# Optimization experiments

Measured on AMD Instinct MI355X. Metric: run time of the kernel, lower is better.

Reference implementation:

```python
import jax, jax.numpy as jnp
import numpy as np

D_MODEL = 1024
NHEAD = 16
HEAD_DIM = D_MODEL // NHEAD
B, S = 4, 2048
NEG_INF = -1000000000.0


def setup_inputs() -> dict:
    key = jax.random.key(0)
    ks = jax.random.split(key, 12)
    s = 1.0 / np.sqrt(D_MODEL)
    inp = {
        "query": jax.random.normal(ks[0], (B, S, D_MODEL), jnp.float32),
        "key": jax.random.normal(ks[1], (B, S, D_MODEL), jnp.float32),
        "value": jax.random.normal(ks[2], (B, S, D_MODEL), jnp.float32),
        # causal mask: 1 = attend, 0 = blocked
        "mask": jnp.broadcast_to(jnp.tril(jnp.ones((S, S), jnp.int32)), (B, S, S)),
        "Wq": jax.random.normal(ks[3], (D_MODEL, D_MODEL), jnp.float32) * s,
        "bq": jnp.zeros((D_MODEL,), jnp.float32),
        "Wk": jax.random.normal(ks[4], (D_MODEL, D_MODEL), jnp.float32) * s,
        "bk": jnp.zeros((D_MODEL,), jnp.float32),
        "Wv": jax.random.normal(ks[5], (D_MODEL, D_MODEL), jnp.float32) * s,
        "bv": jnp.zeros((D_MODEL,), jnp.float32),
        "Wo": jax.random.normal(ks[6], (D_MODEL, D_MODEL), jnp.float32) * s,
        "bo": jnp.zeros((D_MODEL,), jnp.float32),
    }
    return inp


def reference(query, key, value, mask, Wq, bq, Wk, bk, Wv, bv, Wo, bo):
    b, sq, d = query.shape
    scale = np.float32(1.0 / np.sqrt(HEAD_DIM))

    def proj(x, W, bias):
        # nn.Linear: x @ W.T + b, then split heads -> [b, H, s, hd]
        y = jnp.einsum('bsd,ed->bse', x, W) + bias
        return y.reshape(b, -1, NHEAD, HEAD_DIM).transpose(0, 2, 1, 3)

    q = proj(query, Wq, bq)
    k = proj(key, Wk, bk)
    v = proj(value, Wv, bv)

    scores = jnp.einsum('bhqd,bhkd->bhqk', q, k) * scale  # [b,H,sq,sk]
    scores = jnp.where(mask[:, None, :, :] == 0, jnp.float32(NEG_INF), scores)
    attn = jax.nn.softmax(scores, axis=-1)  # dropout p=0 -> identity
    out = jnp.einsum('bhqk,bhkd->bhqd', attn, v)
    out = out.transpose(0, 2, 1, 3).reshape(b, sq, d)
    return jnp.einsum('bsd,ed->bse', out, Wo) + bo
```

## Files before the change

kernel.cpp:

```cpp
#include <hip/hip_runtime.h>
#include <stdint.h>

#define D_MODEL 1024
#define NHEAD   16
#define BATCH   4
#define SEQ     2048
#define M_TOTAL 8192
#define R_ELEMS ((size_t)M_TOTAL * D_MODEL)
#define W_ELEMS ((size_t)D_MODEL * D_MODEL)

typedef short bf8_t __attribute__((ext_vector_type(8)));
typedef float f4_t  __attribute__((ext_vector_type(4)));

#define MFMA16(a, b, c) __builtin_amdgcn_mfma_f32_16x16x32_bf16(a, b, c, 0, 0, 0)

#define SCALE_LOG2E 0.1803368801111244f

#define M_FIX 20.0f

__device__ __forceinline__ unsigned short f2b(float f) {
    union { float f; unsigned int u; } v; v.f = f;
    return (unsigned short)((v.u + 0x7fffu + ((v.u >> 16) & 1u)) >> 16);
}
__device__ __forceinline__ unsigned short f2b_fast(float f) {
    union { float f; unsigned int u; } v; v.f = f;
    return (unsigned short)((v.u + 0x8000u) >> 16);
}

#if __has_builtin(__builtin_amdgcn_exp2f)
#define EXP2(x) __builtin_amdgcn_exp2f(x)
#else
#define EXP2(x) exp2f(x)
#endif

__device__ __forceinline__ void async16(const unsigned short* g, unsigned short* l) {
    __builtin_amdgcn_global_load_lds(
        (const __attribute__((address_space(1))) unsigned int*)g,
        (__attribute__((address_space(3))) unsigned int*)l, 16, 0, 0);
}

__device__ __forceinline__ void cvt_store8(const float* __restrict__ g, unsigned short* l) {
    const float4 x = *(const float4*)g;
    const float4 y = *(const float4*)(g + 4);
    unsigned short t[8] = { f2b(x.x), f2b(x.y), f2b(x.z), f2b(x.w),
                            f2b(y.x), f2b(y.y), f2b(y.z), f2b(y.w) };
    *(uint4*)l = *(const uint4*)t;
}

__global__ __launch_bounds__(256)
void cvt_w(const float* __restrict__ s0, const float* __restrict__ s1,
           const float* __restrict__ s2, const float* __restrict__ s3,
           unsigned short* __restrict__ d) {
    const unsigned int gid = blockIdx.x * 256 + threadIdx.x;
    const unsigned int t = gid >> 17, i = gid & ((1u << 17) - 1);
    const float* s = (t == 0 ? s0 : t == 1 ? s1 : t == 2 ? s2 : s3) + (size_t)i * 8;
    unsigned short* d2 = d + (size_t)t * W_ELEMS + (size_t)i * 8;
    const float4 x = *(const float4*)s;
    const float4 y = *(const float4*)(s + 4);
    unsigned short o[8] = { f2b(x.x), f2b(x.y), f2b(x.z), f2b(x.w),
                            f2b(y.x), f2b(y.y), f2b(y.z), f2b(y.w) };
    *(uint4*)d2 = *(const uint4*)o;
}

template<int AF32, int WF32>
__device__ __forceinline__ void gemm_tile(const void* __restrict__ Ap,
                                          const void* __restrict__ Wp,
                                          const float* __restrict__ bias,
                                          void* __restrict__ outv,
                                          const int ol, const int m0, const int n0,
                                          unsigned short* As, unsigned short* Bs,
                                          const float oscale)
{
    const int tid  = threadIdx.x;
    const int lane = tid & 63;
    const int wave = tid >> 6;
    const int quad = lane >> 4;
    const int l16  = lane & 15;
    const int wm = (wave >> 1) * 64;
    const int wn = (wave & 1) * 64;

    f4_t acc[4][4];
#pragma unroll
    for (int i = 0; i < 4; ++i)
#pragma unroll
        for (int j = 0; j < 4; ++j)
            acc[i][j] = (f4_t){0.f, 0.f, 0.f, 0.f};

    for (int k0 = 0; k0 < 1024; k0 += 64) {
#pragma unroll
        for (int i = 0; i < 4; ++i) {
            const int s = tid + i * 256;
            const int r = s >> 3;
            const int c = (s & 7) ^ (r & 7);
            if (AF32)
                cvt_store8((const float*)Ap + (size_t)(m0 + r) * 1024 + k0 + c * 8, &As[s * 8]);
            else
                async16((const unsigned short*)Ap + (size_t)(m0 + r) * 1024 + k0 + c * 8, &As[s * 8]);
            if (WF32)
                cvt_store8((const float*)Wp + (size_t)(n0 + r) * 1024 + k0 + c * 8, &Bs[s * 8]);
            else
                async16((const unsigned short*)Wp + (size_t)(n0 + r) * 1024 + k0 + c * 8, &Bs[s * 8]);
        }
        __syncthreads();

#pragma unroll
        for (int half = 0; half < 2; ++half) {
            bf8_t af[4], bf[4];
#pragma unroll
            for (int mt = 0; mt < 4; ++mt) {
                const int rr = wm + mt * 16 + l16;
                af[mt] = *(const bf8_t*)&As[(rr * 8 + ((quad + half * 4) ^ (rr & 7))) * 8];
            }
#pragma unroll
            for (int nt = 0; nt < 4; ++nt) {
                const int rr = wn + nt * 16 + l16;
                bf[nt] = *(const bf8_t*)&Bs[(rr * 8 + ((quad + half * 4) ^ (rr & 7))) * 8];
            }
#pragma unroll
            for (int mt = 0; mt < 4; ++mt)
#pragma unroll
                for (int nt = 0; nt < 4; ++nt)
                    acc[mt][nt] = MFMA16(af[mt], bf[nt], acc[mt][nt]);
        }
        __syncthreads();
    }

#pragma unroll
    for (int mt = 0; mt < 4; ++mt) {
#pragma unroll
        for (int nt = 0; nt < 4; ++nt) {
            const int nn = n0 + wn + nt * 16 + l16;
            const float bv = bias[nn];
            const int mbase = m0 + wm + mt * 16 + quad * 4;
            if (ol == 2) {
                float* of = (float*)outv;
#pragma unroll
                for (int r = 0; r < 4; ++r)
                    of[(size_t)(mbase + r) * 1024 + nn] = (acc[mt][nt][r] + bv) * oscale;
            } else if (ol == 0) {
                unsigned short* ob = (unsigned short*)outv;
                const int h = nn >> 6, d = nn & 63;
#pragma unroll
                for (int r = 0; r < 4; ++r) {
                    const int m = mbase + r;
                    const int b = m >> 11, s2 = m & 2047;
                    ob[((size_t)((b * 16 + h) * 2048 + s2) << 6) + d] =
                        f2b((acc[mt][nt][r] + bv) * oscale);
                }
            } else {
                unsigned short* ob = (unsigned short*)outv;
                const int h = nn >> 6, d = nn & 63;
                const int b = mbase >> 11, s2 = mbase & 2047;
                unsigned short pk[4];
#pragma unroll
                for (int r = 0; r < 4; ++r) pk[r] = f2b((acc[mt][nt][r] + bv) * oscale);
                *(uint2*)&ob[((size_t)((b * 16 + h) * 64 + d) << 11) + s2] = *(const uint2*)pk;
            }
        }
    }
}

template<int WF32>
__global__ __launch_bounds__(256, 2)
void qkv_gemm(const float* __restrict__ q_in, const float* __restrict__ k_in,
              const float* __restrict__ v_in,
              const void* __restrict__ Wq, const void* __restrict__ Wk, const void* __restrict__ Wv,
              const float* __restrict__ bq, const float* __restrict__ bk, const float* __restrict__ bv,
              unsigned short* __restrict__ Qh, unsigned short* __restrict__ Kh,
              unsigned short* __restrict__ Vt)
{
    __shared__ unsigned short As[128 * 64];
    __shared__ unsigned short Bs[128 * 64];
    const int z = blockIdx.z;
    const float* A = (z == 0) ? q_in : (z == 1) ? k_in : v_in;
    const void* W  = (z == 0) ? Wq : (z == 1) ? Wk : Wv;
    const float* bias = (z == 0) ? bq : (z == 1) ? bk : bv;
    void* out = (z == 0) ? (void*)Qh : (z == 1) ? (void*)Kh : (void*)Vt;
    gemm_tile<1, WF32>(A, W, bias, out, (z == 2) ? 1 : 0,
                       blockIdx.x * 128, blockIdx.y * 128, As, Bs,
                       (z == 0) ? SCALE_LOG2E : 1.0f);
}

template<int WF32>
__global__ __launch_bounds__(256, 2)
void o_gemm(const unsigned short* __restrict__ ctx, const void* __restrict__ Wo,
            const float* __restrict__ bo, float* __restrict__ out)
{
    __shared__ unsigned short As[128 * 64];
    __shared__ unsigned short Bs[128 * 64];
    gemm_tile<0, WF32>(ctx, Wo, bo, out, 2, blockIdx.x * 128, blockIdx.y * 128, As, Bs, 1.0f);
}

__global__ __launch_bounds__(256, 2)
void attn_kernel(const unsigned short* __restrict__ Qh,
                 const unsigned short* __restrict__ Kh,
                 const unsigned short* __restrict__ Vt,
                 unsigned short* __restrict__ ctx)
{
    __shared__ unsigned short Ks[2][64 * 64];
    __shared__ unsigned short Vs[2][64 * 64];
    __shared__ unsigned short Pw[4][16 * 64];

    const int tid  = threadIdx.x;
    const int lane = tid & 63;
    const int wave = tid >> 6;
    const int quad = lane >> 4;
    const int l16  = lane & 15;

    const int bid = blockIdx.x;
    const int bh  = bid & 63;
    const int jg  = bid >> 6;
    const int j   = jg * 4 + wave;

    const int qrow0[2] = { j * 16, (127 - j) * 16 };
    const int nkt[2] = { (qrow0[0] + 79) >> 6, (qrow0[1] + 79) >> 6 };
    const int nktmax = ((127 - jg * 4) * 16 + 79) >> 6;

    const short ob = (short)0x3F80;
    const bf8_t ONESV = { ob, ob, ob, ob, ob, ob, ob, ob };

    bf8_t qf0[2], qf1[2];
#pragma unroll
    for (int s = 0; s < 2; ++s) {
        const unsigned short* qa = Qh + ((size_t)(bh * SEQ + qrow0[s] + l16) << 6);
        qf0[s] = *(const bf8_t*)(qa + quad * 8);
        qf1[s] = *(const bf8_t*)(qa + 32 + quad * 8);
    }

    f4_t lacc[2];
    f4_t oacc[2][4];
#pragma unroll
    for (int s = 0; s < 2; ++s) {
        lacc[s] = (f4_t){0.f, 0.f, 0.f, 0.f};
#pragma unroll
        for (int r = 0; r < 4; ++r)
            oacc[s][r] = (f4_t){0.f, 0.f, 0.f, 0.f};
    }

    auto stage = [&](int kt2, int bufi) {
        const int kb2 = kt2 * 64;
#pragma unroll
        for (int i2 = 0; i2 < 2; ++i2) {
            const int slot = tid + i2 * 256;
            const int r = slot >> 3;
            const int c = (slot & 7) ^ (r & 7);
            async16(Kh + ((size_t)(bh * SEQ + kb2 + r) << 6) + c * 8, &Ks[bufi][slot * 8]);
            async16(Vt + ((size_t)(bh * 64 + r) << 11) + kb2 + c * 8, &Vs[bufi][slot * 8]);
        }
    };

    stage(0, 0);
    __syncthreads();

    for (int kt = 0; kt < nktmax; ++kt) {
        const int cur = kt & 1;
        if (kt + 1 < nktmax) stage(kt + 1, cur ^ 1);

        const unsigned short* Kc = &Ks[cur][0];
        const unsigned short* Vc = &Vs[cur][0];
        const bool act[2] = { kt < nkt[0], kt < nkt[1] };
        const int kb = kt * 64;

        f4_t sacc[2][4];
#pragma unroll
        for (int nb = 0; nb < 4; ++nb) {
            const int rr = nb * 16 + l16;
            const bf8_t kf0 = *(const bf8_t*)&Kc[(rr * 8 + (quad ^ (rr & 7))) * 8];
            const bf8_t kf1 = *(const bf8_t*)&Kc[(rr * 8 + ((quad + 4) ^ (rr & 7))) * 8];
#pragma unroll
            for (int s = 0; s < 2; ++s) {
                if (!act[s]) continue;
                f4_t sc = (f4_t){-M_FIX, -M_FIX, -M_FIX, -M_FIX};
                sc = MFMA16(kf0, qf0[s], sc);
                sc = MFMA16(kf1, qf1[s], sc);
                sacc[s][nb] = sc;
            }
        }

#pragma unroll
        for (int s = 1; s >= 0; --s) {
            if (!act[s]) continue;
            if (kt == nkt[s] - 1) {
#pragma unroll
                for (int nb = 0; nb < 4; ++nb)
#pragma unroll
                    for (int r = 0; r < 4; ++r)
                        if (kb + nb * 16 + quad * 4 + r > qrow0[s] + l16)
                            sacc[s][nb][r] = -1e30f;
            }

            asm volatile("s_waitcnt lgkmcnt(0)" ::: "memory");

            unsigned short* pws = &Pw[wave][0];
#pragma unroll
            for (int nb = 0; nb < 4; ++nb) {
                const float p0 = EXP2(sacc[s][nb][0]);
                const float p1 = EXP2(sacc[s][nb][1]);
                const float p2 = EXP2(sacc[s][nb][2]);
                const float p3 = EXP2(sacc[s][nb][3]);
                const int c = 2 * nb + (quad >> 1);
                const int eo = l16 * 64 + ((c ^ (l16 & 7)) << 3) + ((quad & 1) << 2);
                unsigned int pklo = __builtin_amdgcn_perm(
                    __float_as_uint(p1) + 0x8000u, __float_as_uint(p0) + 0x8000u, 0x07060302u);
                unsigned int pkhi = __builtin_amdgcn_perm(
                    __float_as_uint(p3) + 0x8000u, __float_as_uint(p2) + 0x8000u, 0x07060302u);
                uint2 pk; pk.x = pklo; pk.y = pkhi;
                *(uint2*)&pws[eo] = pk;
            }

            asm volatile("s_waitcnt lgkmcnt(0)" ::: "memory");

            const bf8_t pf0 = *(const bf8_t*)&pws[(l16 * 8 + (quad ^ (l16 & 7))) * 8];
            const bf8_t pf1 = *(const bf8_t*)&pws[(l16 * 8 + ((quad + 4) ^ (l16 & 7))) * 8];
            lacc[s] = MFMA16(pf0, ONESV, lacc[s]);
            lacc[s] = MFMA16(pf1, ONESV, lacc[s]);
#pragma unroll
            for (int d4 = 0; d4 < 4; ++d4) {
                const int rr = d4 * 16 + l16;
                const bf8_t vfa = *(const bf8_t*)&Vc[(rr * 8 + (quad ^ (rr & 7))) * 8];
                const bf8_t vfb = *(const bf8_t*)&Vc[(rr * 8 + ((quad + 4) ^ (rr & 7))) * 8];
                oacc[s][d4] = MFMA16(pf0, vfa, oacc[s][d4]);
                oacc[s][d4] = MFMA16(pf1, vfb, oacc[s][d4]);
            }
        }
        __syncthreads();
    }

    const int b = bh >> 4, h = bh & 15;
#pragma unroll
    for (int s = 0; s < 2; ++s)
#pragma unroll
        for (int r = 0; r < 4; ++r) {
            const float inv = 1.f / lacc[s][r];
            const int qr = qrow0[s] + quad * 4 + r;
            unsigned short* cb = ctx + ((size_t)(b * SEQ + qr) << 10) + h * 64;
#pragma unroll
            for (int d4 = 0; d4 < 4; ++d4)
                cb[d4 * 16 + l16] = f2b(oacc[s][d4][r] * inv);
        }
}

extern "C" void kernel_launch(void* const* d_in, const int* in_sizes, int n_in,
                              void* d_out, int out_size, void* d_ws, size_t ws_size,
                              hipStream_t stream) {
    const float* q_in = (const float*)d_in[0];
    const float* k_in = (const float*)d_in[1];
    const float* v_in = (const float*)d_in[2];
    const float* Wq = (const float*)d_in[4];
    const float* bq = (const float*)d_in[5];
    const float* Wk = (const float*)d_in[6];
    const float* bk = (const float*)d_in[7];
    const float* Wv = (const float*)d_in[8];
    const float* bv = (const float*)d_in[9];
    const float* Wo = (const float*)d_in[10];
    const float* bo = (const float*)d_in[11];

    unsigned short* w  = (unsigned short*)d_ws;
    unsigned short* Qh = w;
    unsigned short* Kh = w + R_ELEMS;
    unsigned short* Vt = w + 2 * R_ELEMS;
    unsigned short* X  = w + 3 * R_ELEMS;

    const dim3 gb(256);
    const size_t need_big = (4 * R_ELEMS + 4 * W_ELEMS) * 2;

    if (ws_size >= need_big) {
        unsigned short* wb = w + 4 * R_ELEMS;
        cvt_w<<<2048, gb, 0, stream>>>(Wq, Wk, Wv, Wo, wb);
        qkv_gemm<0><<<dim3(64, 8, 3), gb, 0, stream>>>(q_in, k_in, v_in,
                                                       wb, wb + W_ELEMS, wb + 2 * W_ELEMS,
                                                       bq, bk, bv, Qh, Kh, Vt);
        attn_kernel<<<dim3(1024), gb, 0, stream>>>(Qh, Kh, Vt, X);
        o_gemm<0><<<dim3(64, 8), gb, 0, stream>>>(X, wb + 3 * W_ELEMS, bo, (float*)d_out);
    } else {
        qkv_gemm<1><<<dim3(64, 8, 3), gb, 0, stream>>>(q_in, k_in, v_in,
                                                       Wq, Wk, Wv,
                                                       bq, bk, bv, Qh, Kh, Vt);
        attn_kernel<<<dim3(1024), gb, 0, stream>>>(Qh, Kh, Vt, X);
        o_gemm<1><<<dim3(64, 8), gb, 0, stream>>>(X, Wo, bo, (float*)d_out);
    }
}
```

Baseline: 339.9 us.

## Double-buffer GEMM tiles with register-staged fp32 A prefetch and K=32 steps

Restructures the shared GEMM tile loop to double-buffer LDS with a K step of 32 instead of 64. The next tile's fp32 activations are loaded into registers and converted to bf16 into the alternate buffer after the current tile's MFMAs, so global load latency overlaps compute. Only one barrier per iteration remains. The trade-offs are more registers held live for the prefetched values, twice as many loop iterations, and a new 4-chunk XOR swizzle for the LDS layout.

```diff
diff --git a/kernel.cpp b/kernel.cpp
--- a/kernel.cpp
+++ b/kernel.cpp
@@ -22,10 +22,6 @@
     union { float f; unsigned int u; } v; v.f = f;
     return (unsigned short)((v.u + 0x7fffu + ((v.u >> 16) & 1u)) >> 16);
 }
-__device__ __forceinline__ unsigned short f2b_fast(float f) {
-    union { float f; unsigned int u; } v; v.f = f;
-    return (unsigned short)((v.u + 0x8000u) >> 16);
-}
 
 #if __has_builtin(__builtin_amdgcn_exp2f)
 #define EXP2(x) __builtin_amdgcn_exp2f(x)
@@ -37,14 +33,6 @@
     __builtin_amdgcn_global_load_lds(
         (const __attribute__((address_space(1))) unsigned int*)g,
         (__attribute__((address_space(3))) unsigned int*)l, 16, 0, 0);
-}
-
-__device__ __forceinline__ void cvt_store8(const float* __restrict__ g, unsigned short* l) {
-    const float4 x = *(const float4*)g;
-    const float4 y = *(const float4*)(g + 4);
-    unsigned short t[8] = { f2b(x.x), f2b(x.y), f2b(x.z), f2b(x.w),
-                            f2b(y.x), f2b(y.y), f2b(y.z), f2b(y.w) };
-    *(uint4*)l = *(const uint4*)t;
 }
 
 __global__ __launch_bounds__(256)
@@ -86,42 +74,77 @@
         for (int j = 0; j < 4; ++j)
             acc[i][j] = (f4_t){0.f, 0.f, 0.f, 0.f};
 
-    for (int k0 = 0; k0 < 1024; k0 += 64) {
-#pragma unroll
-        for (int i = 0; i < 4; ++i) {
+    float4 a0[2], a1[2];
+
+    auto issue = [&](int k0, int bufi) {
+        unsigned short* Ad = As + bufi * 4096;
+        unsigned short* Bd = Bs + bufi * 4096;
+#pragma unroll
+        for (int i = 0; i < 2; ++i) {
             const int s = tid + i * 256;
-            const int r = s >> 3;
-            const int c = (s & 7) ^ (r & 7);
-            if (AF32)
-                cvt_store8((const float*)Ap + (size_t)(m0 + r) * 1024 + k0 + c * 8, &As[s * 8]);
-            else
-                async16((const unsigned short*)Ap + (size_t)(m0 + r) * 1024 + k0 + c * 8, &As[s * 8]);
-            if (WF32)
-                cvt_store8((const float*)Wp + (size_t)(n0 + r) * 1024 + k0 + c * 8, &Bs[s * 8]);
-            else
-                async16((const unsigned short*)Wp + (size_t)(n0 + r) * 1024 + k0 + c * 8, &Bs[s * 8]);
-        }
-        __syncthreads();
-
-#pragma unroll
-        for (int half = 0; half < 2; ++half) {
-            bf8_t af[4], bf[4];
-#pragma unroll
-            for (int mt = 0; mt < 4; ++mt) {
-                const int rr = wm + mt * 16 + l16;
-                af[mt] = *(const bf8_t*)&As[(rr * 8 + ((quad + half * 4) ^ (rr & 7))) * 8];
-            }
-#pragma unroll
-            for (int nt = 0; nt < 4; ++nt) {
-                const int rr = wn + nt * 16 + l16;
-                bf[nt] = *(const bf8_t*)&Bs[(rr * 8 + ((quad + half * 4) ^ (rr & 7))) * 8];
-            }
-#pragma unroll
-            for (int mt = 0; mt < 4; ++mt)
-#pragma unroll
-                for (int nt = 0; nt < 4; ++nt)
-                    acc[mt][nt] = MFMA16(af[mt], bf[nt], acc[mt][nt]);
-        }
+            const int r = s >> 2;
+            const int c = (s & 3) ^ ((r >> 1) & 3);
+            if (AF32) {
+                const float* g = (const float*)Ap + (size_t)(m0 + r) * 1024 + k0 + c * 8;
+                a0[i] = *(const float4*)g;
+                a1[i] = *(const float4*)(g + 4);
+            } else {
+                async16((const unsigned short*)Ap + (size_t)(m0 + r) * 1024 + k0 + c * 8,
+                        &Ad[s * 8]);
+            }
+            if (WF32) {
+                const float* g = (const float*)Wp + (size_t)(n0 + r) * 1024 + k0 + c * 8;
+                const float4 x = *(const float4*)g;
+                const float4 y = *(const float4*)(g + 4);
+                unsigned short t[8] = { f2b(x.x), f2b(x.y), f2b(x.z), f2b(x.w),
+                                        f2b(y.x), f2b(y.y), f2b(y.z), f2b(y.w) };
+                *(uint4*)&Bd[s * 8] = *(const uint4*)t;
+            } else {
+                async16((const unsigned short*)Wp + (size_t)(n0 + r) * 1024 + k0 + c * 8,
+                        &Bd[s * 8]);
+            }
+        }
+    };
+    auto writeA = [&](int bufi) {
+        if (!AF32) return;
+        unsigned short* Ad = As + bufi * 4096;
+#pragma unroll
+        for (int i = 0; i < 2; ++i) {
+            const int s = tid + i * 256;
+            unsigned short t[8] = { f2b(a0[i].x), f2b(a0[i].y), f2b(a0[i].z), f2b(a0[i].w),
+                                    f2b(a1[i].x), f2b(a1[i].y), f2b(a1[i].z), f2b(a1[i].w) };
+            *(uint4*)&Ad[s * 8] = *(const uint4*)t;
+        }
+    };
+
+    issue(0, 0);
+    writeA(0);
+    __syncthreads();
+
+    for (int kt = 0; kt < 32; ++kt) {
+        const int cur = kt & 1;
+        if (kt + 1 < 32) issue((kt + 1) * 32, cur ^ 1);
+
+        const unsigned short* Ac = As + cur * 4096;
+        const unsigned short* Bc = Bs + cur * 4096;
+        bf8_t af[4], bf[4];
+#pragma unroll
+        for (int mt = 0; mt < 4; ++mt) {
+            const int rr = wm + mt * 16 + l16;
+            af[mt] = *(const bf8_t*)&Ac[(rr * 4 + (quad ^ ((rr >> 1) & 3))) * 8];
+        }
+#pragma unroll
+        for (int nt = 0; nt < 4; ++nt) {
+            const int rr = wn + nt * 16 + l16;
+            bf[nt] = *(const bf8_t*)&Bc[(rr * 4 + (quad ^ ((rr >> 1) & 3))) * 8];
+        }
+#pragma unroll
+        for (int mt = 0; mt < 4; ++mt)
+#pragma unroll
+            for (int nt = 0; nt < 4; ++nt)
+                acc[mt][nt] = MFMA16(af[mt], bf[nt], acc[mt][nt]);
+
+        if (kt + 1 < 32) writeA(cur ^ 1);
         __syncthreads();
     }
 
@@ -169,8 +192,8 @@
               unsigned short* __restrict__ Qh, unsigned short* __restrict__ Kh,
               unsigned short* __restrict__ Vt)
 {
-    __shared__ unsigned short As[128 * 64];
-    __shared__ unsigned short Bs[128 * 64];
+    __shared__ unsigned short As[2 * 128 * 32];
+    __shared__ unsigned short Bs[2 * 128 * 32];
     const int z = blockIdx.z;
     const float* A = (z == 0) ? q_in : (z == 1) ? k_in : v_in;
     const void* W  = (z == 0) ? Wq : (z == 1) ? Wk : Wv;
@@ -186,8 +209,8 @@
 void o_gemm(const unsigned short* __restrict__ ctx, const void* __restrict__ Wo,
             const float* __restrict__ bo, float* __restrict__ out)
 {
-    __shared__ unsigned short As[128 * 64];
-    __shared__ unsigned short Bs[128 * 64];
+    __shared__ unsigned short As[2 * 128 * 32];
+    __shared__ unsigned short Bs[2 * 128 * 32];
     gemm_tile<0, WF32>(ctx, Wo, bo, out, 2, blockIdx.x * 128, blockIdx.y * 128, As, Bs, 1.0f);
 }
 
```

After: 358.3 us. +5.4%, slower.
